# Optimization experiments

Hardware: AMD Instinct MI355X
Metric: run time of the kernel (lower is better)

The kernel has to match this reference:

```python
import jax, jax.numpy as jnp
import numpy as np

SIZE = 512
ATTN = 64      # per-head attention_size
OUT = 64       # per-head output_size
HEADS = 8

def setup_inputs() -> dict:
    key = jax.random.key(0)
    ks = jax.random.split(key, 7)
    s = 0.02
    return {
        "x":  jax.random.normal(ks[0], (4, 2048, SIZE), dtype=jnp.float32),
        "Wq": jax.random.normal(ks[1], (SIZE, ATTN * HEADS), dtype=jnp.float32) * s,
        "bq": jax.random.normal(ks[2], (ATTN * HEADS,), dtype=jnp.float32) * s,
        "Wk": jax.random.normal(ks[3], (SIZE, ATTN), dtype=jnp.float32) * s,  # shared key, no bias
        "Wv": jax.random.normal(ks[4], (SIZE, OUT * HEADS), dtype=jnp.float32) * s,
        "bv": jax.random.normal(ks[5], (OUT * HEADS,), dtype=jnp.float32) * s,
    }

def reference(x, Wq, bq, Wk, Wv, bv):
    B, S, _ = x.shape
    q = (x @ Wq + bq).reshape(B, S, HEADS, ATTN)   # (B,S,H,A)
    k = x @ Wk                                      # (B,S,A) shared across heads
    v = (x @ Wv + bv).reshape(B, S, HEADS, OUT)     # (B,S,H,O)
    # NOTE: original divides by sqrt(seq_len), not sqrt(head_dim)
    scale = 1.0 / np.sqrt(S).astype(np.float32)
    scores = jnp.einsum("bqha,bka->bhqk", q, k) * scale  # (B,H,S,S)
    causal = jnp.tril(jnp.ones((S, S), dtype=bool))
    scores = jnp.where(causal, scores, -jnp.inf)
    attn = jax.nn.softmax(scores, axis=-1)
    out = jnp.einsum("bhqk,bkho->bqho", attn, v)    # (B,S,H,O)
    return out.reshape(B, S, HEADS * OUT)
```

## Files before the change

### kernel.cpp

```cpp
#include <hip/hip_runtime.h>
#include <math.h>


typedef _Float16 half8 __attribute__((ext_vector_type(8)));
typedef _Float16 half4 __attribute__((ext_vector_type(4)));
typedef float float4v __attribute__((ext_vector_type(4)));
typedef unsigned int u32;

#define SCL2E 0.031885926f

__device__ inline float4v mfma16(half8 a, half8 b, float4v c) {
    return __builtin_amdgcn_mfma_f32_16x16x32_f16(a, b, c, 0, 0, 0);
}
__device__ inline void load16(const _Float16* g, _Float16* l) {
    __builtin_amdgcn_global_load_lds((const __attribute__((address_space(1))) u32*)g,
                                     (__attribute__((address_space(3))) u32*)l, 16, 0, 0);
}

__global__ __launch_bounds__(256) void prep(
    const float* __restrict__ x, const float* __restrict__ Wq,
    const float* __restrict__ Wk, const float* __restrict__ Wv,
    _Float16* __restrict__ xh, _Float16* __restrict__ wqt,
    _Float16* __restrict__ wkt, _Float16* __restrict__ wvt) {
    const int bid = blockIdx.x;
    if (bid < 2048) {
        size_t base = (size_t)bid * 2048 + (size_t)threadIdx.x * 8;
        const float4* xp = (const float4*)(x + base);
        float4 f0 = xp[0], f1 = xp[1];
        half8 h = {(_Float16)f0.x, (_Float16)f0.y, (_Float16)f0.z, (_Float16)f0.w,
                   (_Float16)f1.x, (_Float16)f1.y, (_Float16)f1.z, (_Float16)f1.w};
        *(half8*)(xh + base) = h;
    } else {
        int r = bid - 2048;
        const float* W; _Float16* WT; int N, bx, by;
        if (r < 256)      { W = Wq; WT = wqt; N = 512; bx = r & 15; by = r >> 4; }
        else if (r < 288) { r -= 256; W = Wk; WT = wkt; N = 64;  bx = r & 1;  by = r >> 1; }
        else              { r -= 288; W = Wv; WT = wvt; N = 512; bx = r & 15; by = r >> 4; }
        __shared__ float T[32][33];
        const int tx = threadIdx.x & 31, ty = threadIdx.x >> 5;
        const int n0 = bx * 32, k0 = by * 32;
#pragma unroll
        for (int i = 0; i < 4; ++i)
            T[ty + 8 * i][tx] = W[(size_t)(k0 + ty + 8 * i) * N + n0 + tx];
        __syncthreads();
#pragma unroll
        for (int i = 0; i < 4; ++i)
            WT[(size_t)(n0 + ty + 8 * i) * 512 + k0 + tx] = (_Float16)T[tx][ty + 8 * i];
    }
}

__global__ __launch_bounds__(256) void qkv_gemm(
    const _Float16* __restrict__ xh,
    const _Float16* __restrict__ wqt, const _Float16* __restrict__ wkt,
    const _Float16* __restrict__ wvt,
    const float* __restrict__ bq, const float* __restrict__ bv,
    _Float16* __restrict__ q_ws, _Float16* __restrict__ kt_ws, _Float16* __restrict__ vt_ws) {
    __shared__ __align__(16) _Float16 Xs[8192];
    __shared__ __align__(16) _Float16 Ws[4096];

    const int m0 = blockIdx.x * 128;
    const int nt = blockIdx.y;
    const _Float16* WT;
    const float* bias;
    if (nt < 8)       { WT = wqt + (size_t)nt * 64 * 512; bias = bq + nt * 64; }
    else if (nt == 8) { WT = wkt;                          bias = nullptr; }
    else              { WT = wvt + (size_t)(nt - 9) * 64 * 512; bias = bv + (nt - 9) * 64; }

    const int tid = threadIdx.x;
    const int w = tid >> 6, lane = tid & 63, quad = lane >> 4, cl = lane & 15;
    const int lrow = lane >> 3;
    const int lgc = (lane & 7) ^ lrow;
    const _Float16* xg = xh + (size_t)(m0 + lrow) * 512 + lgc * 8;
    const _Float16* wg = WT + (size_t)lrow * 512 + lgc * 8;

    const int g0 = (quad ^ (cl & 7)) << 3;
    const int g1 = ((quad ^ 4) ^ (cl & 7)) << 3;

    float4v acc[2][4] = {};

    for (int ki = 0; ki < 8; ++ki) {
        const int kk = ki * 64;
        __syncthreads();
#pragma unroll
        for (int c = 0; c < 4; ++c) {
            int cc = w * 4 + c;
            load16(xg + (size_t)cc * 8 * 512 + kk, Xs + cc * 512);
        }
#pragma unroll
        for (int c = 0; c < 2; ++c) {
            int cc = w * 2 + c;
            load16(wg + (size_t)cc * 8 * 512 + kk, Ws + cc * 512);
        }
        __syncthreads();
#pragma unroll
        for (int c = 0; c < 2; ++c) {
            const int g = c ? g1 : g0;
#pragma unroll
            for (int s = 0; s < 2; ++s) {
                half8 a = *(const half8*)(Xs + (w * 32 + s * 16 + cl) * 64 + g);
#pragma unroll
                for (int j = 0; j < 4; ++j) {
                    half8 b = *(const half8*)(Ws + (j * 16 + cl) * 64 + g);
                    acc[s][j] = mfma16(a, b, acc[s][j]);
                }
            }
        }
    }

    if (nt < 8) {
#pragma unroll
        for (int s = 0; s < 2; ++s)
#pragma unroll
            for (int j = 0; j < 4; ++j)
#pragma unroll
                for (int r = 0; r < 4; ++r) {
                    int lr = w * 32 + s * 16 + quad * 4 + r;
                    int col = j * 16 + cl;
                    q_ws[(size_t)(m0 + lr) * 512 + nt * 64 + col] =
                        (_Float16)((acc[s][j][r] + bias[col]) * SCL2E);
                }
    } else if (nt == 8) {
#pragma unroll
        for (int s = 0; s < 2; ++s)
#pragma unroll
            for (int j = 0; j < 4; ++j)
#pragma unroll
                for (int r = 0; r < 4; ++r) {
                    int grow = m0 + w * 32 + s * 16 + quad * 4 + r;
                    int b = grow >> 11, t = (grow >> 6) & 31, row = grow & 63;
                    int col = j * 16 + cl;
                    kt_ws[((size_t)(b * 32 + t) << 12) + row * 64 +
                          (((col >> 3) ^ (row & 7)) << 3) + (col & 7)] = (_Float16)acc[s][j][r];
                }
    } else {
        const int h = nt - 9;
#pragma unroll
        for (int s = 0; s < 2; ++s)
#pragma unroll
            for (int j = 0; j < 4; ++j)
#pragma unroll
                for (int r = 0; r < 4; ++r) {
                    int grow = m0 + w * 32 + s * 16 + quad * 4 + r;
                    int b = grow >> 11, t = (grow >> 6) & 31, row = grow & 63;
                    int o = j * 16 + cl;
                    int kap = ((row & 15) << 2) + (row >> 4);
                    vt_ws[(((size_t)(b * 8 + h) * 32 + t) << 12) + o * 64 +
                          (((kap >> 3) ^ (o & 7)) << 3) + (kap & 7)] =
                        (_Float16)(acc[s][j][r] + bias[o]);
                }
    }
}

__global__ __launch_bounds__(256) void attn(
    const _Float16* __restrict__ q_ws, const _Float16* __restrict__ kt_ws,
    const _Float16* __restrict__ vt_ws, float* __restrict__ out) {
    __shared__ __align__(16) _Float16 Ks[4096];
    __shared__ __align__(16) _Float16 VTs[2][4096];
    __shared__ __align__(16) _Float16 Ps[4][1024];

    const int bh = blockIdx.x, b = bh >> 3, h = bh & 7;
    const int pair = blockIdx.y;
    const int bS = b * 2048;
    const int tid = threadIdx.x;
    const int w = tid >> 6, lane = tid & 63, quad = lane >> 4, cl = lane & 15;

    const _Float16* kbase = kt_ws + ((size_t)(b * 32) << 12);
    const _Float16* vbase = vt_ws + ((size_t)((b * 8 + h) * 32) << 12);

    const int g0 = (quad ^ (cl & 7)) << 3;
    const int g1 = ((quad ^ 4) ^ (cl & 7)) << 3;
    const int soff = w * 1024 + lane * 8;

    for (int phase = 0; phase < 2; ++phase) {
        const int qt = phase ? (31 - pair) : pair;
        const int tlast = qt;
        const int q0 = qt * 64;

        const _Float16* qbase = q_ws + (size_t)(bS + q0 + w * 16 + cl) * 512 + h * 64;
        half8 qa0 = *(const half8*)(qbase + quad * 8);
        half8 qa1 = *(const half8*)(qbase + 32 + quad * 8);

        float4v oacc[4] = {};
        float l_run[4] = {0.f, 0.f, 0.f, 0.f};

        __syncthreads();
        load16(kbase + soff,       &Ks[w * 1024]);
        load16(kbase + soff + 512, &Ks[w * 1024 + 512]);
        load16(vbase + soff,       &VTs[0][w * 1024]);
        load16(vbase + soff + 512, &VTs[0][w * 1024 + 512]);

        for (int t = 0; t <= tlast; ++t) {
            __syncthreads();
            if (t < tlast) {
                const _Float16* vg = vbase + ((size_t)(t + 1) << 12);
                const int nb = (t + 1) & 1;
                load16(vg + soff,       &VTs[nb][w * 1024]);
                load16(vg + soff + 512, &VTs[nb][w * 1024 + 512]);
            }
            const bool diag = (t == tlast);
            const int jmax = diag ? w : 3;

            float4v sfr[4];
#pragma unroll
            for (int j = 0; j < 4; ++j) {
                if (j <= jmax) {
                    const _Float16* kr = &Ks[(j * 16 + cl) * 64];
                    half8 b0 = *(const half8*)(kr + g0);
                    half8 b1 = *(const half8*)(kr + g1);
                    float4v a_ = {0.f, 0.f, 0.f, 0.f};
                    a_ = mfma16(qa0, b0, a_);
                    a_ = mfma16(qa1, b1, a_);
                    sfr[j] = a_;
                }
            }
#pragma unroll
            for (int r = 0; r < 4; ++r) {
                float pj[4];
#pragma unroll
                for (int j = 0; j < 4; ++j) {
                    bool live = (j < jmax) || ((j == jmax) && (!diag || cl <= quad * 4 + r));
                    pj[j] = live ? exp2f(sfr[j][r]) : 0.f;
                }
                l_run[r] += (pj[0] + pj[1]) + (pj[2] + pj[3]);
                int rr = quad * 4 + r;
                half4 ph = {(_Float16)pj[0], (_Float16)pj[1], (_Float16)pj[2], (_Float16)pj[3]};
                *(half4*)&Ps[w][rr * 64 + ((((cl >> 1) ^ (rr & 7)) << 3) | ((cl & 1) << 2))] = ph;
            }
            __syncthreads();
            if (t < tlast) {
                const _Float16* kg = kbase + ((size_t)(t + 1) << 12);
                load16(kg + soff,       &Ks[w * 1024]);
                load16(kg + soff + 512, &Ks[w * 1024 + 512]);
            }
            const _Float16* PB = &Ps[w][cl * 64];
            half8 pa0 = *(const half8*)(PB + g0);
            half8 pa1 = *(const half8*)(PB + g1);
            const int bb = t & 1;
#pragma unroll
            for (int jo = 0; jo < 4; ++jo) {
                const _Float16* vr = &VTs[bb][(jo * 16 + cl) * 64];
                half8 v0 = *(const half8*)(vr + g0);
                half8 v1 = *(const half8*)(vr + g1);
                oacc[jo] = mfma16(pa0, v0, oacc[jo]);
                oacc[jo] = mfma16(pa1, v1, oacc[jo]);
            }
        }
#pragma unroll
        for (int r = 0; r < 4; ++r) {
            float l = l_run[r];
            l += __shfl_xor(l, 1);
            l += __shfl_xor(l, 2);
            l += __shfl_xor(l, 4);
            l += __shfl_xor(l, 8);
            float inv = 1.0f / l;
            int row = q0 + w * 16 + quad * 4 + r;
            float* op = out + (size_t)(bS + row) * 512 + h * 64 + cl;
            op[0]  = oacc[0][r] * inv;
            op[16] = oacc[1][r] * inv;
            op[32] = oacc[2][r] * inv;
            op[48] = oacc[3][r] * inv;
        }
    }
}

extern "C" void kernel_launch(void* const* d_in, const int* in_sizes, int n_in,
                              void* d_out, int out_size, void* d_ws, size_t ws_size,
                              hipStream_t stream) {
    const float* x  = (const float*)d_in[0];
    const float* Wq = (const float*)d_in[1];
    const float* bq = (const float*)d_in[2];
    const float* Wk = (const float*)d_in[3];
    const float* Wv = (const float*)d_in[4];
    const float* bv = (const float*)d_in[5];
    float* out = (float*)d_out;

    char* ws = (char*)d_ws;
    _Float16* q_ws  = (_Float16*)(ws);
    _Float16* kt_ws = (_Float16*)(ws + 8388608);
    _Float16* vt_ws = (_Float16*)(ws + 9437184);
    _Float16* wqt   = (_Float16*)(ws + 17825792);
    _Float16* wkt   = (_Float16*)(ws + 18350080);
    _Float16* wvt   = (_Float16*)(ws + 18415616);
    _Float16* xh    = (_Float16*)(ws + 18939904);

    prep<<<dim3(2592), dim3(256), 0, stream>>>(x, Wq, Wk, Wv, xh, wqt, wkt, wvt);

    qkv_gemm<<<dim3(64, 17), dim3(256), 0, stream>>>(
        xh, wqt, wkt, wvt, bq, bv, q_ws, kt_ws, vt_ws);

    attn<<<dim3(32, 16), dim3(256), 0, stream>>>(q_ws, kt_ws, vt_ws, out);
}
```

Baseline: 162.3 us.

## Widen QKV GEMM tiles, stage epilogue via LDS, split attention per tile

The QKV GEMM now computes 128-column output tiles, giving 9 column blocks instead of 17, so each X tile loaded from global is reused across twice as many columns. Its epilogue writes results into shared memory in the target swizzled layout and then stores them with coalesced 16-byte writes, replacing scattered 2-byte stores. The attention kernel drops the paired short/long q-tile scheme for one q-tile per block over a 32x32 grid, and double-buffers K as well as V so there is one barrier per iteration instead of two. The costs are higher register and LDS use in the GEMM and possible load imbalance between causal tiles of different lengths in attention.

```diff
diff --git a/kernel.cpp b/kernel.cpp
--- a/kernel.cpp
+++ b/kernel.cpp
@@ -55,16 +55,18 @@
     const _Float16* __restrict__ wvt,
     const float* __restrict__ bq, const float* __restrict__ bv,
     _Float16* __restrict__ q_ws, _Float16* __restrict__ kt_ws, _Float16* __restrict__ vt_ws) {
-    __shared__ __align__(16) _Float16 Xs[8192];
-    __shared__ __align__(16) _Float16 Ws[4096];
+    __shared__ __align__(16) _Float16 SB[16384];
+    _Float16* Xs = SB;
+    _Float16* Ws2 = SB + 8192;
+    _Float16* Cs = SB;
 
     const int m0 = blockIdx.x * 128;
     const int nt = blockIdx.y;
     const _Float16* WT;
-    const float* bias;
-    if (nt < 8)       { WT = wqt + (size_t)nt * 64 * 512; bias = bq + nt * 64; }
-    else if (nt == 8) { WT = wkt;                          bias = nullptr; }
-    else              { WT = wvt + (size_t)(nt - 9) * 64 * 512; bias = bv + (nt - 9) * 64; }
+    int wchunks, nj;
+    if (nt < 4)      { WT = wqt + (size_t)nt * 128 * 512;       wchunks = 16; nj = 8; }
+    else if (nt < 8) { WT = wvt + (size_t)(nt - 4) * 128 * 512; wchunks = 16; nj = 8; }
+    else             { WT = wkt;                                 wchunks = 8;  nj = 4; }
 
     const int tid = threadIdx.x;
     const int w = tid >> 6, lane = tid & 63, quad = lane >> 4, cl = lane & 15;
@@ -76,7 +78,7 @@
     const int g0 = (quad ^ (cl & 7)) << 3;
     const int g1 = ((quad ^ 4) ^ (cl & 7)) << 3;
 
-    float4v acc[2][4] = {};
+    float4v acc[2][8] = {};
 
     for (int ki = 0; ki < 8; ++ki) {
         const int kk = ki * 64;
@@ -87,80 +89,108 @@
             load16(xg + (size_t)cc * 8 * 512 + kk, Xs + cc * 512);
         }
 #pragma unroll
-        for (int c = 0; c < 2; ++c) {
-            int cc = w * 2 + c;
-            load16(wg + (size_t)cc * 8 * 512 + kk, Ws + cc * 512);
+        for (int c = 0; c < 4; ++c) {
+            int cc = w * 4 + c;
+            if (cc < wchunks)
+                load16(wg + (size_t)cc * 8 * 512 + kk, Ws2 + cc * 512);
         }
         __syncthreads();
 #pragma unroll
         for (int c = 0; c < 2; ++c) {
             const int g = c ? g1 : g0;
-#pragma unroll
-            for (int s = 0; s < 2; ++s) {
-                half8 a = *(const half8*)(Xs + (w * 32 + s * 16 + cl) * 64 + g);
-#pragma unroll
-                for (int j = 0; j < 4; ++j) {
-                    half8 b = *(const half8*)(Ws + (j * 16 + cl) * 64 + g);
-                    acc[s][j] = mfma16(a, b, acc[s][j]);
+            half8 a0 = *(const half8*)(Xs + (w * 32 + cl) * 64 + g);
+            half8 a1 = *(const half8*)(Xs + (w * 32 + 16 + cl) * 64 + g);
+#pragma unroll
+            for (int j = 0; j < 8; ++j) {
+                if (j < nj) {
+                    half8 b = *(const half8*)(Ws2 + (j * 16 + cl) * 64 + g);
+                    acc[0][j] = mfma16(a0, b, acc[0][j]);
+                    acc[1][j] = mfma16(a1, b, acc[1][j]);
                 }
             }
         }
     }
 
-    if (nt < 8) {
+    __syncthreads();
+    const int b = m0 >> 11, t0 = (m0 >> 6) & 31;
+    if (nt < 4) {
+        const float* bias = bq + nt * 128;
 #pragma unroll
         for (int s = 0; s < 2; ++s)
 #pragma unroll
+            for (int j = 0; j < 8; ++j)
+#pragma unroll
+                for (int r = 0; r < 4; ++r) {
+                    int row = w * 32 + s * 16 + quad * 4 + r;
+                    int col = j * 16 + cl;
+                    Cs[row * 128 + col] = (_Float16)((acc[s][j][r] + bias[col]) * SCL2E);
+                }
+        __syncthreads();
+#pragma unroll
+        for (int p = 0; p < 8; ++p) {
+            int idx = p * 2048 + tid * 8;
+            int row = idx >> 7, col = idx & 127;
+            *(half8*)(q_ws + (size_t)(m0 + row) * 512 + nt * 128 + col) = *(const half8*)(Cs + idx);
+        }
+    } else if (nt < 8) {
+        const float* bias = bv + (nt - 4) * 128;
+#pragma unroll
+        for (int s = 0; s < 2; ++s)
+#pragma unroll
+            for (int j = 0; j < 8; ++j)
+#pragma unroll
+                for (int r = 0; r < 4; ++r) {
+                    int row = w * 32 + s * 16 + quad * 4 + r;
+                    int col = j * 16 + cl;
+                    int hh = col >> 6, o = col & 63;
+                    int kap = ((row & 15) << 2) + ((row >> 4) & 3);
+                    Cs[hh * 8192 + (row >> 6) * 4096 + o * 64 +
+                       ((((kap >> 3) ^ (o & 7)) << 3) | (kap & 7))] =
+                        (_Float16)(acc[s][j][r] + bias[col]);
+                }
+        __syncthreads();
+#pragma unroll
+        for (int p = 0; p < 8; ++p) {
+            int idx = p * 2048 + tid * 8;
+            int blob = idx >> 12;
+            int hh = blob >> 1, rt = blob & 1;
+            _Float16* ob = vt_ws + (((size_t)(b * 8 + (nt - 4) * 2 + hh) * 32 + t0 + rt) << 12);
+            *(half8*)(ob + (idx & 4095)) = *(const half8*)(Cs + idx);
+        }
+    } else {
+#pragma unroll
+        for (int s = 0; s < 2; ++s)
+#pragma unroll
             for (int j = 0; j < 4; ++j)
 #pragma unroll
                 for (int r = 0; r < 4; ++r) {
-                    int lr = w * 32 + s * 16 + quad * 4 + r;
+                    int row = w * 32 + s * 16 + quad * 4 + r;
                     int col = j * 16 + cl;
-                    q_ws[(size_t)(m0 + lr) * 512 + nt * 64 + col] =
-                        (_Float16)((acc[s][j][r] + bias[col]) * SCL2E);
+                    Cs[(row >> 6) * 4096 + (row & 63) * 64 +
+                       ((((col >> 3) ^ (row & 7)) << 3) | (col & 7))] = (_Float16)acc[s][j][r];
                 }
-    } else if (nt == 8) {
-#pragma unroll
-        for (int s = 0; s < 2; ++s)
-#pragma unroll
-            for (int j = 0; j < 4; ++j)
-#pragma unroll
-                for (int r = 0; r < 4; ++r) {
-                    int grow = m0 + w * 32 + s * 16 + quad * 4 + r;
-                    int b = grow >> 11, t = (grow >> 6) & 31, row = grow & 63;
-                    int col = j * 16 + cl;
-                    kt_ws[((size_t)(b * 32 + t) << 12) + row * 64 +
-                          (((col >> 3) ^ (row & 7)) << 3) + (col & 7)] = (_Float16)acc[s][j][r];
-                }
-    } else {
-        const int h = nt - 9;
-#pragma unroll
-        for (int s = 0; s < 2; ++s)
-#pragma unroll
-            for (int j = 0; j < 4; ++j)
-#pragma unroll
-                for (int r = 0; r < 4; ++r) {
-                    int grow = m0 + w * 32 + s * 16 + quad * 4 + r;
-                    int b = grow >> 11, t = (grow >> 6) & 31, row = grow & 63;
-                    int o = j * 16 + cl;
-                    int kap = ((row & 15) << 2) + (row >> 4);
-                    vt_ws[(((size_t)(b * 8 + h) * 32 + t) << 12) + o * 64 +
-                          (((kap >> 3) ^ (o & 7)) << 3) + (kap & 7)] =
-                        (_Float16)(acc[s][j][r] + bias[o]);
-                }
+        __syncthreads();
+#pragma unroll
+        for (int p = 0; p < 4; ++p) {
+            int idx = p * 2048 + tid * 8;
+            int rt = idx >> 12;
+            _Float16* ob = kt_ws + ((size_t)(b * 32 + t0 + rt) << 12);
+            *(half8*)(ob + (idx & 4095)) = *(const half8*)(Cs + idx);
+        }
     }
 }
 
 __global__ __launch_bounds__(256) void attn(
     const _Float16* __restrict__ q_ws, const _Float16* __restrict__ kt_ws,
     const _Float16* __restrict__ vt_ws, float* __restrict__ out) {
-    __shared__ __align__(16) _Float16 Ks[4096];
+    __shared__ __align__(16) _Float16 Ks[2][4096];
     __shared__ __align__(16) _Float16 VTs[2][4096];
     __shared__ __align__(16) _Float16 Ps[4][1024];
 
     const int bh = blockIdx.x, b = bh >> 3, h = bh & 7;
-    const int pair = blockIdx.y;
-    const int bS = b * 2048;
+    const int qt = 31 - (int)blockIdx.y;
+    const int tlast = qt;
+    const int q0 = qt * 64, bS = b * 2048;
     const int tid = threadIdx.x;
     const int w = tid >> 6, lane = tid & 63, quad = lane >> 4, cl = lane & 15;
 
@@ -171,95 +201,84 @@
     const int g1 = ((quad ^ 4) ^ (cl & 7)) << 3;
     const int soff = w * 1024 + lane * 8;
 
-    for (int phase = 0; phase < 2; ++phase) {
-        const int qt = phase ? (31 - pair) : pair;
-        const int tlast = qt;
-        const int q0 = qt * 64;
-
-        const _Float16* qbase = q_ws + (size_t)(bS + q0 + w * 16 + cl) * 512 + h * 64;
-        half8 qa0 = *(const half8*)(qbase + quad * 8);
-        half8 qa1 = *(const half8*)(qbase + 32 + quad * 8);
-
-        float4v oacc[4] = {};
-        float l_run[4] = {0.f, 0.f, 0.f, 0.f};
-
-        __syncthreads();
-        load16(kbase + soff,       &Ks[w * 1024]);
-        load16(kbase + soff + 512, &Ks[w * 1024 + 512]);
-        load16(vbase + soff,       &VTs[0][w * 1024]);
-        load16(vbase + soff + 512, &VTs[0][w * 1024 + 512]);
-
-        for (int t = 0; t <= tlast; ++t) {
-            __syncthreads();
-            if (t < tlast) {
-                const _Float16* vg = vbase + ((size_t)(t + 1) << 12);
-                const int nb = (t + 1) & 1;
-                load16(vg + soff,       &VTs[nb][w * 1024]);
-                load16(vg + soff + 512, &VTs[nb][w * 1024 + 512]);
+    const _Float16* qbase = q_ws + (size_t)(bS + q0 + w * 16 + cl) * 512 + h * 64;
+    half8 qa0 = *(const half8*)(qbase + quad * 8);
+    half8 qa1 = *(const half8*)(qbase + 32 + quad * 8);
+
+    float4v oacc[4] = {};
+    float l_run[4] = {0.f, 0.f, 0.f, 0.f};
+
+    load16(kbase + soff,       &Ks[0][soff]);
+    load16(kbase + soff + 512, &Ks[0][soff + 512]);
+    load16(vbase + soff,       &VTs[0][soff]);
+    load16(vbase + soff + 512, &VTs[0][soff + 512]);
+
+    for (int t = 0; t <= tlast; ++t) {
+        __syncthreads();
+        if (t < tlast) {
+            const size_t off = (size_t)(t + 1) << 12;
+            const int nb = (t + 1) & 1;
+            load16(kbase + off + soff,       &Ks[nb][soff]);
+            load16(kbase + off + soff + 512, &Ks[nb][soff + 512]);
+            load16(vbase + off + soff,       &VTs[nb][soff]);
+            load16(vbase + off + soff + 512, &VTs[nb][soff + 512]);
+        }
+        const int bb = t & 1;
+        const bool diag = (t == tlast);
+        const int jmax = diag ? w : 3;
+
+        float4v sfr[4];
+#pragma unroll
+        for (int j = 0; j < 4; ++j) {
+            if (j <= jmax) {
+                const _Float16* kr = &Ks[bb][(j * 16 + cl) * 64];
+                half8 b0 = *(const half8*)(kr + g0);
+                half8 b1 = *(const half8*)(kr + g1);
+                float4v a_ = {0.f, 0.f, 0.f, 0.f};
+                a_ = mfma16(qa0, b0, a_);
+                a_ = mfma16(qa1, b1, a_);
+                sfr[j] = a_;
             }
-            const bool diag = (t == tlast);
-            const int jmax = diag ? w : 3;
-
-            float4v sfr[4];
+        }
+#pragma unroll
+        for (int r = 0; r < 4; ++r) {
+            float pj[4];
 #pragma unroll
             for (int j = 0; j < 4; ++j) {
-                if (j <= jmax) {
-                    const _Float16* kr = &Ks[(j * 16 + cl) * 64];
-                    half8 b0 = *(const half8*)(kr + g0);
-                    half8 b1 = *(const half8*)(kr + g1);
-                    float4v a_ = {0.f, 0.f, 0.f, 0.f};
-                    a_ = mfma16(qa0, b0, a_);
-                    a_ = mfma16(qa1, b1, a_);
-                    sfr[j] = a_;
-                }
+                bool live = (j < jmax) || ((j == jmax) && (!diag || cl <= quad * 4 + r));
+                pj[j] = live ? exp2f(sfr[j][r]) : 0.f;
             }
-#pragma unroll
-            for (int r = 0; r < 4; ++r) {
-                float pj[4];
-#pragma unroll
-                for (int j = 0; j < 4; ++j) {
-                    bool live = (j < jmax) || ((j == jmax) && (!diag || cl <= quad * 4 + r));
-                    pj[j] = live ? exp2f(sfr[j][r]) : 0.f;
-                }
-                l_run[r] += (pj[0] + pj[1]) + (pj[2] + pj[3]);
-                int rr = quad * 4 + r;
-                half4 ph = {(_Float16)pj[0], (_Float16)pj[1], (_Float16)pj[2], (_Float16)pj[3]};
-                *(half4*)&Ps[w][rr * 64 + ((((cl >> 1) ^ (rr & 7)) << 3) | ((cl & 1) << 2))] = ph;
-            }
-            __syncthreads();
-            if (t < tlast) {
-                const _Float16* kg = kbase + ((size_t)(t + 1) << 12);
-                load16(kg + soff,       &Ks[w * 1024]);
-                load16(kg + soff + 512, &Ks[w * 1024 + 512]);
-            }
-            const _Float16* PB = &Ps[w][cl * 64];
-            half8 pa0 = *(const half8*)(PB + g0);
-            half8 pa1 = *(const half8*)(PB + g1);
-            const int bb = t & 1;
-#pragma unroll
-            for (int jo = 0; jo < 4; ++jo) {
-                const _Float16* vr = &VTs[bb][(jo * 16 + cl) * 64];
-                half8 v0 = *(const half8*)(vr + g0);
-                half8 v1 = *(const half8*)(vr + g1);
-                oacc[jo] = mfma16(pa0, v0, oacc[jo]);
-                oacc[jo] = mfma16(pa1, v1, oacc[jo]);
-            }
-        }
-#pragma unroll
-        for (int r = 0; r < 4; ++r) {
-            float l = l_run[r];
-            l += __shfl_xor(l, 1);
-            l += __shfl_xor(l, 2);
-            l += __shfl_xor(l, 4);
-            l += __shfl_xor(l, 8);
-            float inv = 1.0f / l;
-            int row = q0 + w * 16 + quad * 4 + r;
-            float* op = out + (size_t)(bS + row) * 512 + h * 64 + cl;
-            op[0]  = oacc[0][r] * inv;
-            op[16] = oacc[1][r] * inv;
-            op[32] = oacc[2][r] * inv;
-            op[48] = oacc[3][r] * inv;
-        }
+            l_run[r] += (pj[0] + pj[1]) + (pj[2] + pj[3]);
+            int rr = quad * 4 + r;
+            half4 ph = {(_Float16)pj[0], (_Float16)pj[1], (_Float16)pj[2], (_Float16)pj[3]};
+            *(half4*)&Ps[w][rr * 64 + ((((cl >> 1) ^ (rr & 7)) << 3) | ((cl & 1) << 2))] = ph;
+        }
+        const _Float16* PB = &Ps[w][cl * 64];
+        half8 pa0 = *(const half8*)(PB + g0);
+        half8 pa1 = *(const half8*)(PB + g1);
+#pragma unroll
+        for (int jo = 0; jo < 4; ++jo) {
+            const _Float16* vr = &VTs[bb][(jo * 16 + cl) * 64];
+            half8 v0 = *(const half8*)(vr + g0);
+            half8 v1 = *(const half8*)(vr + g1);
+            oacc[jo] = mfma16(pa0, v0, oacc[jo]);
+            oacc[jo] = mfma16(pa1, v1, oacc[jo]);
+        }
+    }
+#pragma unroll
+    for (int r = 0; r < 4; ++r) {
+        float l = l_run[r];
+        l += __shfl_xor(l, 1);
+        l += __shfl_xor(l, 2);
+        l += __shfl_xor(l, 4);
+        l += __shfl_xor(l, 8);
+        float inv = 1.0f / l;
+        int row = q0 + w * 16 + quad * 4 + r;
+        float* op = out + (size_t)(bS + row) * 512 + h * 64 + cl;
+        op[0]  = oacc[0][r] * inv;
+        op[16] = oacc[1][r] * inv;
+        op[32] = oacc[2][r] * inv;
+        op[48] = oacc[3][r] * inv;
     }
 }
 
@@ -285,8 +304,8 @@
 
     prep<<<dim3(2592), dim3(256), 0, stream>>>(x, Wq, Wk, Wv, xh, wqt, wkt, wvt);
 
-    qkv_gemm<<<dim3(64, 17), dim3(256), 0, stream>>>(
+    qkv_gemm<<<dim3(64, 9), dim3(256), 0, stream>>>(
         xh, wqt, wkt, wvt, bq, bv, q_ws, kt_ws, vt_ws);
 
-    attn<<<dim3(32, 16), dim3(256), 0, stream>>>(q_ws, kt_ws, vt_ws, out);
-}
+    attn<<<dim3(32, 32), dim3(256), 0, stream>>>(q_ws, kt_ws, vt_ws, out);
+}
```

Result: faster. 157.4 us (-3.0%).
